# Performance work log

Hardware: AMD Instinct MI355X
Metric: run time of the kernel (lower is better)

Reference implementation:

```python
import jax, jax.numpy as jnp
import numpy as np

B, NF, H = 1024, 64, 512


def setup_inputs() -> dict:
    key = jax.random.key(0)
    ks = jax.random.split(key, 12)
    sc_in2 = 1.0 / np.sqrt(2 * H)
    sc_in1 = 1.0 / np.sqrt(H)
    inp = {
        "field_vectors": jax.random.normal(ks[0], (B, NF, H), dtype=jnp.float32),
        # and_fusion: Linear(2H->H), ReLU, Linear(H->H)
        "and_W1": jax.random.uniform(ks[1], (2 * H, H), jnp.float32, -sc_in2, sc_in2),
        "and_b1": jax.random.uniform(ks[2], (H,), jnp.float32, -sc_in2, sc_in2),
        "and_W2": jax.random.uniform(ks[3], (H, H), jnp.float32, -sc_in1, sc_in1),
        "and_b2": jax.random.uniform(ks[4], (H,), jnp.float32, -sc_in1, sc_in1),
        # or_fusion: Linear(2H->H), ReLU, Linear(H->H)
        "or_W1": jax.random.uniform(ks[5], (2 * H, H), jnp.float32, -sc_in2, sc_in2),
        "or_b1": jax.random.uniform(ks[6], (H,), jnp.float32, -sc_in2, sc_in2),
        "or_W2": jax.random.uniform(ks[7], (H, H), jnp.float32, -sc_in1, sc_in1),
        "or_b2": jax.random.uniform(ks[8], (H,), jnp.float32, -sc_in1, sc_in1),
        # not_transform: Linear(H->H), Tanh
        "not_W": jax.random.uniform(ks[9], (H, H), jnp.float32, -sc_in1, sc_in1),
        "not_b": jax.random.uniform(ks[10], (H,), jnp.float32, -sc_in1, sc_in1),
        # Disjoint index structure so the torch skip-set logic is a no-op:
        # 'and' pairs use fields 0..31, 'or' pairs use 32..47, leftovers 48..63.
        "not_idx": 48 + jnp.arange(8, dtype=jnp.int32),
        "and_pairs": jnp.arange(32, dtype=jnp.int32).reshape(16, 2),
        "or_pairs": (32 + jnp.arange(16, dtype=jnp.int32)).reshape(8, 2),
        "leftover_idx": 48 + jnp.arange(16, dtype=jnp.int32),
    }
    return inp


def _mlp2(x, W1, b1, W2, b2):
    # Linear -> ReLU -> Linear
    return jax.nn.relu(x @ W1 + b1) @ W2 + b2


def reference(field_vectors, and_W1, and_b1, and_W2, and_b2,
              or_W1, or_b1, or_W2, or_b2, not_W, not_b,
              not_idx, and_pairs, or_pairs, leftover_idx):
    # In-place 'not' transform on selected fields (Tanh(Linear))
    fv = field_vectors.at[:, not_idx].set(
        jnp.tanh(field_vectors[:, not_idx] @ not_W + not_b))
    # Gather (i, j) pairs, concat along feature dim -> [B, P, 2H]
    cat_and = jnp.concatenate([fv[:, and_pairs[:, 0]], fv[:, and_pairs[:, 1]]], axis=-1)
    fused_and = _mlp2(cat_and, and_W1, and_b1, and_W2, and_b2)  # [B, 16, H]
    cat_or = jnp.concatenate([fv[:, or_pairs[:, 0]], fv[:, or_pairs[:, 1]]], axis=-1)
    fused_or = _mlp2(cat_or, or_W1, or_b1, or_W2, or_b2)  # [B, 8, H]
    # Stack order matches torch loop: and results, or results, untouched fields
    return jnp.concatenate([fused_and, fused_or, fv[:, leftover_idx]], axis=1)
```

## Files before the change

### kernel.cpp

```cpp
#include <hip/hip_runtime.h>
#include <hip/hip_bf16.h>
#include <math.h>

typedef __attribute__((ext_vector_type(8))) __bf16 bf16x8;
typedef __attribute__((ext_vector_type(4))) float f32x4;

__device__ __forceinline__ unsigned short f2bf(float f) {
    union { float f; unsigned u; } v; v.f = f;
    unsigned r = v.u + 0x7fffu + ((v.u >> 16) & 1u);
    return (unsigned short)(r >> 16);
}
__device__ __forceinline__ unsigned int pk(float a, float b) {
    union { float f; unsigned u; } x, y; x.f = a; y.f = b;
    unsigned ra = (x.u + 0x7fffu + ((x.u >> 16) & 1u)) >> 16;
    unsigned rb = (y.u + 0x7fffu + ((y.u >> 16) & 1u)) & 0xffff0000u;
    return ra | rb;
}

__device__ __forceinline__ void gl2lds16(const unsigned short* g, unsigned short* l) {
    __builtin_amdgcn_global_load_lds(
        (const __attribute__((address_space(1))) unsigned int*)(g),
        (__attribute__((address_space(3))) unsigned int*)(l), 16, 0, 0);
}

struct SetupArgs {
    const int *and_pairs, *or_pairs, *not_idx, *lidx;
    int* tbl;
    const float* W[5];
    unsigned short* WT[5];
    int K[5], N[5];
    int tstart[6];
};

__global__ __launch_bounds__(256) void setup_kernel(SetupArgs a) {
    __shared__ float tile[64][65];
    const int blk = blockIdx.x;
    const int tid = threadIdx.x;

    if (blk == 0) {
        if (tid < 64) {
            const int f = tid;
            int u = 0;
            for (int i = 0; i < 32; i++) u |= (a.and_pairs[i] == f);
            for (int i = 0; i < 16; i++) u |= (a.or_pairs[i] == f);
            int isnot = 0;
            for (int i = 0; i < 8; i++)  isnot |= (a.not_idx[i] == f);
            int ls = -1;
            for (int l = 0; l < 16; l++) if (a.lidx[l] == f) ls = l;
            if (isnot) ls = -1;
            a.tbl[f] = (u | isnot) | ((ls + 1) << 8);
        }
        return;
    }

    const int bx = blk - 1;
    int m = 0;
    while (bx >= a.tstart[m + 1]) m++;
    const float* src = a.W[m];
    unsigned short* dst = a.WT[m];
    const int K = a.K[m], N = a.N[m];
    const int t = bx - a.tstart[m];
    const int ntn = N >> 6;
    const int tk = t / ntn, tn = t % ntn;
    const int c = tid & 63, r0 = tid >> 6;
    #pragma unroll
    for (int r = r0; r < 64; r += 4)
        tile[r][c] = src[(size_t)(tk * 64 + r) * N + tn * 64 + c];
    __syncthreads();
    #pragma unroll
    for (int r = r0; r < 64; r += 4)
        dst[(size_t)(tn * 64 + r) * K + tk * 64 + c] = f2bf(tile[c][r]);
}

struct PrepArgs {
    const float* fv;
    unsigned short* fvb;
    const int* tbl;
    float* out;
};

__global__ __launch_bounds__(256) void prep_kernel(PrepArgs a) {
    const int t = blockIdx.x * 256 + threadIdx.x;
    const size_t e = (size_t)t * 8;
    const int c = (int)(e & 511);
    const int f = (int)((e >> 9) & 63);
    const int b = (int)(e >> 15);
    const float4 v0 = *(const float4*)(a.fv + e);
    const float4 v1 = *(const float4*)(a.fv + e + 4);
    const int tb = a.tbl[f];
    const int u  = tb & 0xff;
    const int ls = (tb >> 8) - 1;
    if (u) {
        uint4 o;
        o.x = pk(v0.x, v0.y); o.y = pk(v0.z, v0.w);
        o.z = pk(v1.x, v1.y); o.w = pk(v1.z, v1.w);
        ((uint4*)a.fvb)[t] = o;
    }
    if (ls >= 0) {
        float* d = a.out + ((size_t)b * 40 + 24 + ls) * 512 + c;
        *(float4*)(d)     = v0;
        *(float4*)(d + 4) = v1;
    }
}

#define LOADB(DST, WTP, KD, K0)                                              \
    _Pragma("unroll") for (int ni = 0; ni < 8; ni++)                         \
        DST[ni] = *(const bf16x8*)((WTP) +                                   \
            (size_t)(wn + ni * 16 + ln15) * (KD) + (K0) + kq * 8);

#define MMAC(BF, AF)                                                         \
    _Pragma("unroll") for (int mi = 0; mi < 4; mi++)                         \
    _Pragma("unroll") for (int ni = 0; ni < 8; ni++)                         \
        acc[mi][ni] = __builtin_amdgcn_mfma_f32_16x16x32_bf16(               \
            AF[mi], BF[ni], acc[mi][ni], 0, 0, 0);

template <int P, int K1, int SRCM, int PATH, int QBASE>
__device__ __forceinline__ void fused_seg(
    const unsigned short* __restrict__ A,
    const int* __restrict__ idx,
    const unsigned short* __restrict__ W1T,
    const float* __restrict__ b1,
    const unsigned short* __restrict__ W2T,
    const float* __restrict__ b2,
    float* __restrict__ out,
    const int* __restrict__ leftover,
    int local,
    unsigned short* As, unsigned short* hid) {

    const int tid  = threadIdx.x;
    const int lane = tid & 63, w = tid >> 6;
    const int ln15 = lane & 15;
    const int kq   = lane >> 4;
    const int wn   = w * 128;
    const int m0   = local * 64;

    const int skin = ((lane & 3) ^ ((lane >> 2) & 3)) * 8;
    const unsigned short *ar0, *ar1;
    {
        const int m = m0 + w * 16 + (lane >> 2);
        if constexpr (SRCM == 0) {
            const int b = m / P, p = m % P;
            ar0 = A + ((size_t)b * 64 + idx[2 * p]) * 512;
            ar1 = A + ((size_t)b * 64 + idx[2 * p + 1]) * 512;
        } else {
            const int b = m >> 3, i = m & 7;
            ar0 = A + ((size_t)b * 64 + idx[i]) * 512;
            ar1 = ar0;
        }
    }
    auto stageA = [&](int buf, int t) {
        const int k0 = t * 32;
        const unsigned short* src;
        if constexpr (SRCM == 0)
            src = (k0 >= 512 ? ar1 + (k0 - 512) : ar0 + k0) + skin;
        else
            src = ar0 + k0 + skin;
        gl2lds16(src, &As[buf * 2048 + w * 512]);
    };
    const int xsel = (kq ^ (lane & 3)) * 8;

    f32x4 acc[4][8];
    #pragma unroll
    for (int mi = 0; mi < 4; mi++)
        #pragma unroll
        for (int ni = 0; ni < 8; ni++)
            acc[mi][ni] = f32x4{0.f, 0.f, 0.f, 0.f};

    bf16x8 bA[8], bB[8];

    constexpr int NT1 = K1 / 32;
    stageA(0, 0);
    LOADB(bA, W1T, K1, 0);
    __syncthreads();
    for (int t = 0; t < NT1; t += 2) {
        stageA(1, t + 1);
        bf16x8 af[4];
        #pragma unroll
        for (int mi = 0; mi < 4; mi++)
            af[mi] = *(const bf16x8*)&As[(mi * 16 + ln15) * 32 + xsel];
        LOADB(bB, W1T, K1, (t + 1) * 32);
        MMAC(bA, af);
        __syncthreads();
        if (t + 2 < NT1) stageA(0, t + 2);
        #pragma unroll
        for (int mi = 0; mi < 4; mi++)
            af[mi] = *(const bf16x8*)&As[2048 + (mi * 16 + ln15) * 32 + xsel];
        if (t + 2 < NT1) { LOADB(bA, W1T, K1, (t + 2) * 32); }
        MMAC(bB, af);
        __syncthreads();
    }

    if constexpr (PATH == 2) {
        int qmap[8];
        #pragma unroll
        for (int i = 0; i < 8; i++) {
            const int f = idx[i];
            int q = 24;
            for (int l = 0; l < 16; l++)
                if (leftover[l] == f) q = 24 + l;
            qmap[i] = q;
        }
        #pragma unroll
        for (int ni = 0; ni < 8; ni++) {
            const int n = wn + ni * 16 + ln15;
            const float bv = b1[n];
            #pragma unroll
            for (int mi = 0; mi < 4; mi++)
                #pragma unroll
                for (int j = 0; j < 4; j++) {
                    const int r = mi * 16 + kq * 4 + j;
                    const int m = m0 + r;
                    const int b = m >> 3, i = m & 7;
                    out[((size_t)b * 40 + qmap[i]) * 512 + n] =
                        tanhf(acc[mi][ni][j] + bv);
                }
        }
        return;
    }

    #pragma unroll
    for (int ni = 0; ni < 8; ni++) {
        const int n  = wn + ni * 16 + ln15;
        const float bv = b1[n];
        const int c8 = n >> 3;
        const int cl = (n & 7) * 2;
        #pragma unroll
        for (int mi = 0; mi < 4; mi++)
            #pragma unroll
            for (int j = 0; j < 4; j++) {
                const int r = mi * 16 + kq * 4 + j;
                float v = acc[mi][ni][j] + bv;
                v = v > 0.f ? v : 0.f;
                *(unsigned short*)((char*)hid + r * 1024 +
                                   ((c8 ^ (r & 7)) * 16) + cl) = f2bf(v);
            }
    }
    #pragma unroll
    for (int mi = 0; mi < 4; mi++)
        #pragma unroll
        for (int ni = 0; ni < 8; ni++)
            acc[mi][ni] = f32x4{0.f, 0.f, 0.f, 0.f};
    LOADB(bA, W2T, 512, 0);
    __syncthreads();

    for (int t2 = 0; t2 < 16; t2 += 2) {
        bf16x8 af[4];
        #pragma unroll
        for (int mi = 0; mi < 4; mi++) {
            const int r = mi * 16 + ln15;
            const int c8 = t2 * 4 + kq;
            af[mi] = *(const bf16x8*)((char*)hid + r * 1024 +
                                      ((c8 ^ (r & 7)) * 16));
        }
        LOADB(bB, W2T, 512, (t2 + 1) * 32);
        MMAC(bA, af);
        #pragma unroll
        for (int mi = 0; mi < 4; mi++) {
            const int r = mi * 16 + ln15;
            const int c8 = (t2 + 1) * 4 + kq;
            af[mi] = *(const bf16x8*)((char*)hid + r * 1024 +
                                      ((c8 ^ (r & 7)) * 16));
        }
        if (t2 + 2 < 16) { LOADB(bA, W2T, 512, (t2 + 2) * 32); }
        MMAC(bB, af);
    }

    #pragma unroll
    for (int ni = 0; ni < 8; ni++) {
        const int n  = wn + ni * 16 + ln15;
        const float bv = b2[n];
        #pragma unroll
        for (int mi = 0; mi < 4; mi++)
            #pragma unroll
            for (int j = 0; j < 4; j++) {
                const int r = mi * 16 + kq * 4 + j;
                const int m = m0 + r;
                const int b = m / P, p = m % P;
                out[((size_t)b * 40 + QBASE + p) * 512 + n] =
                    acc[mi][ni][j] + bv;
            }
    }
}

struct FArgs {
    const unsigned short *fvb, *and_W1T, *and_W2T, *or_W1T, *or_W2T, *not_WT;
    const int *and_pairs, *or_pairs, *not_idx, *leftover;
    const float *and_b1, *and_b2, *or_b1, *or_b2, *not_b;
    float* out;
};

__global__ __launch_bounds__(256, 2) void fused_phase(FArgs a) {
    __shared__ __align__(16) unsigned short As[2 * 64 * 32];
    __shared__ __align__(16) unsigned short hid[64 * 512];
    const int blk = blockIdx.x;
    if (blk < 256)
        fused_seg<16, 1024, 0, 0, 0>(a.fvb, a.and_pairs, a.and_W1T, a.and_b1,
                                     a.and_W2T, a.and_b2, a.out, nullptr,
                                     blk, As, hid);
    else if (blk < 384)
        fused_seg<8, 1024, 0, 0, 16>(a.fvb, a.or_pairs, a.or_W1T, a.or_b1,
                                     a.or_W2T, a.or_b2, a.out, nullptr,
                                     blk - 256, As, hid);
    else
        fused_seg<8, 512, 1, 2, 24>(a.fvb, a.not_idx, a.not_WT, a.not_b,
                                    nullptr, nullptr, a.out, a.leftover,
                                    blk - 384, As, hid);
}

extern "C" void kernel_launch(void* const* d_in, const int* in_sizes, int n_in,
                              void* d_out, int out_size, void* d_ws, size_t ws_size,
                              hipStream_t stream) {
    const float* fv       = (const float*)d_in[0];
    const float* and_W1   = (const float*)d_in[1];
    const float* and_b1   = (const float*)d_in[2];
    const float* and_W2   = (const float*)d_in[3];
    const float* and_b2   = (const float*)d_in[4];
    const float* or_W1    = (const float*)d_in[5];
    const float* or_b1    = (const float*)d_in[6];
    const float* or_W2    = (const float*)d_in[7];
    const float* or_b2    = (const float*)d_in[8];
    const float* not_W    = (const float*)d_in[9];
    const float* not_b    = (const float*)d_in[10];
    const int* not_idx    = (const int*)d_in[11];
    const int* and_pairs  = (const int*)d_in[12];
    const int* or_pairs   = (const int*)d_in[13];
    const int* leftover   = (const int*)d_in[14];
    float* out = (float*)d_out;
    char* ws = (char*)d_ws;

    unsigned short* fvb     = (unsigned short*)(ws);
    unsigned short* and_W1T = (unsigned short*)(ws + 67108864);
    unsigned short* or_W1T  = (unsigned short*)(ws + 68157440);
    unsigned short* and_W2T = (unsigned short*)(ws + 69206016);
    unsigned short* or_W2T  = (unsigned short*)(ws + 69730304);
    unsigned short* not_WT  = (unsigned short*)(ws + 70254592);
    int*            tbl     = (int*)(ws + 70778880);

    SetupArgs sa;
    sa.and_pairs = and_pairs; sa.or_pairs = or_pairs;
    sa.not_idx = not_idx; sa.lidx = leftover; sa.tbl = tbl;
    sa.W[0] = and_W1; sa.WT[0] = and_W1T; sa.K[0] = 1024; sa.N[0] = 512;
    sa.W[1] = or_W1;  sa.WT[1] = or_W1T;  sa.K[1] = 1024; sa.N[1] = 512;
    sa.W[2] = and_W2; sa.WT[2] = and_W2T; sa.K[2] = 512;  sa.N[2] = 512;
    sa.W[3] = or_W2;  sa.WT[3] = or_W2T;  sa.K[3] = 512;  sa.N[3] = 512;
    sa.W[4] = not_W;  sa.WT[4] = not_WT;  sa.K[4] = 512;  sa.N[4] = 512;
    sa.tstart[0] = 0;   sa.tstart[1] = 128; sa.tstart[2] = 256;
    sa.tstart[3] = 320; sa.tstart[4] = 384; sa.tstart[5] = 448;
    setup_kernel<<<dim3(449), dim3(256), 0, stream>>>(sa);

    PrepArgs pa;
    pa.fv = fv; pa.fvb = fvb; pa.tbl = tbl; pa.out = out;
    prep_kernel<<<dim3(16384), dim3(256), 0, stream>>>(pa);

    FArgs fa;
    fa.fvb = fvb;
    fa.and_W1T = and_W1T; fa.and_W2T = and_W2T;
    fa.or_W1T = or_W1T;   fa.or_W2T = or_W2T;   fa.not_WT = not_WT;
    fa.and_pairs = and_pairs; fa.or_pairs = or_pairs; fa.not_idx = not_idx;
    fa.leftover = leftover;
    fa.and_b1 = and_b1; fa.and_b2 = and_b2;
    fa.or_b1 = or_b1;   fa.or_b2 = or_b2;   fa.not_b = not_b;
    fa.out = out;
    fused_phase<<<dim3(512), dim3(256), 0, stream>>>(fa);
}
```

Measured before the change: 359.4 us.

## Deepen A-tile LDS pipeline to four buffers with partial vmcnt barriers

```diff
diff --git a/kernel.cpp b/kernel.cpp
--- a/kernel.cpp
+++ b/kernel.cpp
@@ -114,6 +114,10 @@
         acc[mi][ni] = __builtin_amdgcn_mfma_f32_16x16x32_bf16(               \
             AF[mi], BF[ni], acc[mi][ni], 0, 0, 0);
 
+#define L1BAR()                                                              \
+    asm volatile("s_waitcnt vmcnt(9) lgkmcnt(0)" ::: "memory");              \
+    asm volatile("s_barrier" ::: "memory");
+
 template <int P, int K1, int SRCM, int PATH, int QBASE>
 __device__ __forceinline__ void fused_seg(
     const unsigned short* __restrict__ A,
@@ -170,24 +174,32 @@
 
     constexpr int NT1 = K1 / 32;
     stageA(0, 0);
+    stageA(1, 1);
+    __builtin_amdgcn_sched_barrier(0);
     LOADB(bA, W1T, K1, 0);
-    __syncthreads();
-    for (int t = 0; t < NT1; t += 2) {
-        stageA(1, t + 1);
+
+    for (int h = 0; h < NT1; h += 2) {
+        L1BAR();
+        if (h + 2 < NT1) stageA((h + 2) & 3, h + 2);
+        __builtin_amdgcn_sched_barrier(0);
+        LOADB(bB, W1T, K1, (h + 1) * 32);
         bf16x8 af[4];
         #pragma unroll
         for (int mi = 0; mi < 4; mi++)
-            af[mi] = *(const bf16x8*)&As[(mi * 16 + ln15) * 32 + xsel];
-        LOADB(bB, W1T, K1, (t + 1) * 32);
+            af[mi] = *(const bf16x8*)&As[(h & 3) * 2048 +
+                                         (mi * 16 + ln15) * 32 + xsel];
         MMAC(bA, af);
-        __syncthreads();
-        if (t + 2 < NT1) stageA(0, t + 2);
+        __builtin_amdgcn_sched_barrier(0);
+        L1BAR();
+        if (h + 3 < NT1) stageA((h + 3) & 3, h + 3);
+        __builtin_amdgcn_sched_barrier(0);
+        if (h + 2 < NT1) { LOADB(bA, W1T, K1, (h + 2) * 32); }
         #pragma unroll
         for (int mi = 0; mi < 4; mi++)
-            af[mi] = *(const bf16x8*)&As[2048 + (mi * 16 + ln15) * 32 + xsel];
-        if (t + 2 < NT1) { LOADB(bA, W1T, K1, (t + 2) * 32); }
+            af[mi] = *(const bf16x8*)&As[((h + 1) & 3) * 2048 +
+                                         (mi * 16 + ln15) * 32 + xsel];
         MMAC(bB, af);
-        __syncthreads();
+        __builtin_amdgcn_sched_barrier(0);
     }
 
     if constexpr (PATH == 2) {
@@ -290,7 +302,7 @@
 };
 
 __global__ __launch_bounds__(256, 2) void fused_phase(FArgs a) {
-    __shared__ __align__(16) unsigned short As[2 * 64 * 32];
+    __shared__ __align__(16) unsigned short As[4 * 64 * 32];
     __shared__ __align__(16) unsigned short hid[64 * 512];
     const int blk = blockIdx.x;
     if (blk < 256)
```

New measurement: 372.7 us. 1.04x slower.
